# Performance work log

Measured on AMD Instinct MI355X. Metric: run time of the kernel, lower is better.

## Reference

```python
import jax, jax.numpy as jnp
import numpy as np

NORM = 20.0   # from dataset 'NETS'
ALPHA = 1.0
EPS = 1e-12   # torch F.normalize eps


def _l2_normalize(x):
    n = jnp.sqrt(jnp.sum(x * x, axis=-1, keepdims=True))
    return x / jnp.maximum(n, EPS)


def setup_inputs() -> dict:
    key = jax.random.key(0)
    k1, k2, k3, k4, k5 = jax.random.split(key, 5)
    B, P, C = 4096, 32, 512
    predicted_score = jax.random.uniform(k1, (B,), dtype=jnp.float32) * NORM
    targets = jax.random.uniform(k2, (B,), dtype=jnp.float32) * NORM
    feats = jax.random.normal(k3, (B, C), dtype=jnp.float32)
    pivot_features = jax.random.normal(k4, (B, P, C), dtype=jnp.float32)
    pivot_scores = jax.random.uniform(k5, (B, P), dtype=jnp.float32) * NORM
    return {
        "predicted_score": predicted_score,
        "targets": targets,
        "feats": feats,
        "pivot_features": pivot_features,
        "pivot_scores": pivot_scores,
    }


def reference(predicted_score, targets, feats, pivot_features, pivot_scores):
    scale = ALPHA * NORM
    f = _l2_normalize(feats)                      # (B, C)
    pf = _l2_normalize(pivot_features)            # (B, P, C)
    ps = pivot_scores.astype(jnp.float32)         # (B, P)

    # image-text: (B,1,C) @ (B,C,P) -> (B,P)
    it_matches = jnp.einsum('bc,bpc->bp', f, pf)
    it_label = 1.0 - 2.0 * jnp.abs(targets[:, None] - ps) / scale
    image_text_loss = jnp.mean(jnp.abs(it_matches - it_label))

    # image-image: (B,B)
    ii_matches = f @ f.T
    ii_label = 1.0 - 2.0 * jnp.abs(targets[:, None] - targets[None, :]) / scale
    image_image_loss = jnp.mean(jnp.abs(ii_matches - ii_label))

    # text-text: (B,P,P)
    tt_matches = jnp.einsum('bpc,bqc->bpq', pf, pf)
    tt_label = 1.0 - 2.0 * jnp.abs(ps[:, :, None] - ps[:, None, :]) / scale
    text_text_loss = jnp.mean(jnp.abs(tt_matches - tt_label))

    mae_loss = jnp.mean(jnp.abs(predicted_score - targets))

    return (image_image_loss, text_text_loss, image_text_loss, mae_loss)
```

## Files before the change

### kernel.cpp

```cpp
#include <hip/hip_runtime.h>
#include <hip/hip_bf16.h>
#include <stdint.h>

#define B_N 4096
#define P_N 32
#define C_N 512
#define LABC 0.1f
#define N_II 528
#define GRID_TOTAL (N_II * 9)
#define N_TT (GRID_TOTAL - N_II)

typedef float  floatx4 __attribute__((ext_vector_type(4)));
typedef __bf16 bf16x8  __attribute__((ext_vector_type(8)));

__device__ __forceinline__ unsigned short f2bf(float x) {
    return __builtin_bit_cast(unsigned short, __float2bfloat16(x));
}
__device__ __forceinline__ uint4 pack8(const float4& v0, const float4& v1) {
    uint4 pk;
    pk.x = (unsigned)f2bf(v0.x) | ((unsigned)f2bf(v0.y) << 16);
    pk.y = (unsigned)f2bf(v0.z) | ((unsigned)f2bf(v0.w) << 16);
    pk.z = (unsigned)f2bf(v1.x) | ((unsigned)f2bf(v1.y) << 16);
    pk.w = (unsigned)f2bf(v1.z) | ((unsigned)f2bf(v1.w) << 16);
    return pk;
}
__device__ __forceinline__ void bfly_reduce2(float& a, float& b) {
#pragma unroll
    for (int m = 1; m < 64; m <<= 1) {
        a += __shfl_xor(a, m, 64);
        b += __shfl_xor(b, m, 64);
    }
}
__device__ __forceinline__ void bfly_reduce1(float& a) {
#pragma unroll
    for (int m = 1; m < 64; m <<= 1) a += __shfl_xor(a, m, 64);
}

__global__ __launch_bounds__(256) void k_prep(const float* __restrict__ feats,
                                              const float* __restrict__ pred,
                                              const float* __restrict__ targ,
                                              unsigned short* __restrict__ fb,
                                              float* __restrict__ maePart) {
    const int wave = threadIdx.x >> 6, lane = threadIdx.x & 63;
    const int row = blockIdx.x * 4 + wave;
    const float* src = feats + (size_t)row * C_N + lane * 8;
    float4 v0 = *(const float4*)src;
    float4 v1 = *(const float4*)(src + 4);
    float ss = v0.x*v0.x + v0.y*v0.y + v0.z*v0.z + v0.w*v0.w
             + v1.x*v1.x + v1.y*v1.y + v1.z*v1.z + v1.w*v1.w;
    bfly_reduce1(ss);
    const float inv = rsqrtf(fmaxf(ss, 1e-24f));
    float4 n0 = {v0.x*inv, v0.y*inv, v0.z*inv, v0.w*inv};
    float4 n1 = {v1.x*inv, v1.y*inv, v1.z*inv, v1.w*inv};
    *(uint4*)(fb + (size_t)row * C_N + lane * 8) = pack8(n0, n1);

    if (wave == 0) {
        float v = 0.f;
        if (lane < 4) {
            const int r = blockIdx.x * 4 + lane;
            v = fabsf(pred[r] - targ[r]);
        }
        v += __shfl_xor(v, 1, 64);
        v += __shfl_xor(v, 2, 64);
        if (lane == 0) maePart[blockIdx.x] = v;
    }
}

#define APAD 130
struct TTsm {
    unsigned short pfs[64 * 33 * 8];
    float psS[P_N];
    float rdiag[P_N];
    float redT[4], redI[4];
};
struct IIsm {
    unsigned short As[4 * APAD * 8];
    unsigned short Bs[4 * APAD * 8];
    float tm[128], tn[128];
    float red[4];
};
union SMu { TTsm tt; IIsm ii; };

__global__ __launch_bounds__(256) void k_fused(const float* __restrict__ pf_g,
                                               const float* __restrict__ ps_g,
                                               const float* __restrict__ targets,
                                               const unsigned short* __restrict__ fb,
                                               double* __restrict__ partII,
                                               double* __restrict__ partTT,
                                               double* __restrict__ partIT) {
    __shared__ __align__(16) SMu sm;
    const int tid = threadIdx.x, wave = tid >> 6, lane = tid & 63;
    const int quad = lane >> 4, l15 = lane & 15;
    const int bid = blockIdx.x;
    const bool isII = (bid % 9) == 0;

    if (isII) {
        IIsm& S = sm.ii;
        int bm = 0, rem = bid / 9;
        while (rem >= 32 - bm) { rem -= 32 - bm; ++bm; }
        const int bn = bm + rem;
        const int wr = wave >> 1, wc = wave & 1;
        const int mbase = bm * 128, nbase = bn * 128;

        if (tid < 128) S.tm[tid] = targets[mbase + tid];
        else           S.tn[tid - 128] = targets[nbase + tid - 128];

        const int row = tid >> 1, half = tid & 1;
        const unsigned short* aSrc = fb + (size_t)(mbase + row) * C_N + half * 16;
        const unsigned short* bSrc = fb + (size_t)(nbase + row) * C_N + half * 16;
        const int c0 = half * 2, c1 = half * 2 + 1;

        floatx4 accv[16];
#pragma unroll
        for (int i = 0; i < 16; ++i) accv[i] = (floatx4){0.f, 0.f, 0.f, 0.f};

        uint4 a0 = *(const uint4*)(aSrc);
        uint4 a1 = *(const uint4*)(aSrc + 8);
        uint4 b0 = *(const uint4*)(bSrc);
        uint4 b1 = *(const uint4*)(bSrc + 8);

        for (int ks = 0; ks < 16; ++ks) {
            __syncthreads();
            *(uint4*)&S.As[((size_t)c0 * APAD + row) * 8] = a0;
            *(uint4*)&S.As[((size_t)c1 * APAD + row) * 8] = a1;
            *(uint4*)&S.Bs[((size_t)c0 * APAD + row) * 8] = b0;
            *(uint4*)&S.Bs[((size_t)c1 * APAD + row) * 8] = b1;
            __syncthreads();
            if (ks < 15) {
                const int off = (ks + 1) * 32;
                a0 = *(const uint4*)(aSrc + off);
                a1 = *(const uint4*)(aSrc + off + 8);
                b0 = *(const uint4*)(bSrc + off);
                b1 = *(const uint4*)(bSrc + off + 8);
            }
            bf16x8 af[4], bfv[4];
#pragma unroll
            for (int t = 0; t < 4; ++t)
                af[t] = __builtin_bit_cast(bf16x8, *(const uint4*)&S.As[((size_t)quad * APAD + wr * 64 + t * 16 + l15) * 8]);
#pragma unroll
            for (int t = 0; t < 4; ++t)
                bfv[t] = __builtin_bit_cast(bf16x8, *(const uint4*)&S.Bs[((size_t)quad * APAD + wc * 64 + t * 16 + l15) * 8]);
#pragma unroll
            for (int ti = 0; ti < 4; ++ti)
#pragma unroll
                for (int tj = 0; tj < 4; ++tj)
                    accv[ti * 4 + tj] = __builtin_amdgcn_mfma_f32_16x16x32_bf16(af[ti], bfv[tj], accv[ti * 4 + tj], 0, 0, 0);
        }

        float s = 0.f;
#pragma unroll
        for (int ti = 0; ti < 4; ++ti)
#pragma unroll
            for (int tj = 0; tj < 4; ++tj)
#pragma unroll
                for (int r = 0; r < 4; ++r) {
                    const int p = wr * 64 + ti * 16 + quad * 4 + r;
                    const int q = wc * 64 + tj * 16 + l15;
                    const float lab = 1.f - LABC * fabsf(S.tm[p] - S.tn[q]);
                    s += fabsf(accv[ti * 4 + tj][r] - lab);
                }
        if (bm != bn) s *= 2.f;
        bfly_reduce1(s);
        if (lane == 0) S.red[wave] = s;
        __syncthreads();
        if (tid == 0) partII[bid / 9] = (double)(S.red[0] + S.red[1] + S.red[2] + S.red[3]);
    } else {
        const int b = bid - (bid / 9) - 1;
        TTsm& S = sm.tt;
        if (b >= B_N) {
            if (tid == 0) { partTT[b] = 0.0; partIT[b] = 0.0; }
            return;
        }

        const float* base = pf_g + (size_t)b * P_N * C_N;
        uint4 st[16];
#pragma unroll
        for (int i = 0; i < 8; ++i) {
            const float* src = base + (wave * 8 + i) * C_N + lane * 8;
            st[2 * i]     = *(const uint4*)src;
            st[2 * i + 1] = *(const uint4*)(src + 4);
        }
        uint4 fReg = {0u, 0u, 0u, 0u};
        if (wave == 0) fReg = *(const uint4*)(fb + (size_t)b * C_N + lane * 8);
        if (tid < P_N) S.psS[tid] = ps_g[b * P_N + tid];
        const float tb = targets[b];

#pragma unroll
        for (int i = 0; i < 8; ++i) {
            const int r = wave * 8 + i;
            const float4 v0 = __builtin_bit_cast(float4, st[2 * i]);
            const float4 v1 = __builtin_bit_cast(float4, st[2 * i + 1]);
            *(uint4*)&S.pfs[((size_t)lane * 33 + r) * 8] = pack8(v0, v1);
        }
        if (wave == 0) *(uint4*)&S.pfs[((size_t)lane * 33 + 32) * 8] = fReg;
        __syncthreads();

        const int pt = (wave >> 1) * 16, qt = (wave & 1) * 16;
        const bool doF = (wave < 2);
        floatx4 acc4 = {0.f, 0.f, 0.f, 0.f};
        floatx4 accF = {0.f, 0.f, 0.f, 0.f};
        const uint4 zero4 = {0u, 0u, 0u, 0u};
#pragma unroll
        for (int kk = 0; kk < 16; ++kk) {
            const int ch = kk * 4 + quad;
            bf16x8 a = __builtin_bit_cast(bf16x8, *(const uint4*)&S.pfs[((size_t)ch * 33 + pt + l15) * 8]);
            bf16x8 bb = __builtin_bit_cast(bf16x8, *(const uint4*)&S.pfs[((size_t)ch * 33 + qt + l15) * 8]);
            acc4 = __builtin_amdgcn_mfma_f32_16x16x32_bf16(a, bb, acc4, 0, 0, 0);
            if (doF) {
                uint4 fr = *(const uint4*)&S.pfs[((size_t)ch * 33 + 32) * 8];
                bf16x8 af = __builtin_bit_cast(bf16x8, (l15 == 0) ? fr : zero4);
                accF = __builtin_amdgcn_mfma_f32_16x16x32_bf16(af, bb, accF, 0, 0, 0);
            }
        }
        if (pt == qt) {
            if ((l15 >> 2) == quad) S.rdiag[pt + l15] = rsqrtf(fmaxf(acc4[l15 & 3], 1e-24f));
        }
        __syncthreads();

        float tt_sum = 0.f, it_sum = 0.f;
#pragma unroll
        for (int r = 0; r < 4; ++r) {
            const int p = pt + quad * 4 + r;
            const int q = qt + l15;
            const float val = acc4[r] * S.rdiag[p] * S.rdiag[q];
            const float lab = 1.f - LABC * fabsf(S.psS[p] - S.psS[q]);
            tt_sum += fabsf(val - lab);
        }
        if (doF && quad == 0) {
            const int q = qt + l15;
            const float val = accF[0] * S.rdiag[q];
            const float lab = 1.f - LABC * fabsf(tb - S.psS[q]);
            it_sum = fabsf(val - lab);
        }
        bfly_reduce2(tt_sum, it_sum);
        if (lane == 0) { S.redT[wave] = tt_sum; S.redI[wave] = it_sum; }
        __syncthreads();
        if (tid == 0) {
            partTT[b] = (double)(S.redT[0] + S.redT[1] + S.redT[2] + S.redT[3]);
            partIT[b] = (double)(S.redI[0] + S.redI[1] + S.redI[2] + S.redI[3]);
        }
    }
}

__global__ __launch_bounds__(256) void k_final(const double* __restrict__ partII,
                                               const double* __restrict__ partTT,
                                               const double* __restrict__ partIT,
                                               const float* __restrict__ maePart,
                                               float* __restrict__ out) {
    __shared__ double redA[4], redB[4], redC[4];
    __shared__ float redM[4];
    const int tid = threadIdx.x, wave = tid >> 6, lane = tid & 63;

    double sII = 0.0, sTT = 0.0, sIT = 0.0;
    for (int i = tid; i < N_II; i += 256) sII += partII[i];
    for (int i = tid; i < N_TT; i += 256) { sTT += partTT[i]; sIT += partIT[i]; }
    float sM = maePart[tid] + maePart[tid + 256] + maePart[tid + 512] + maePart[tid + 768];

#pragma unroll
    for (int m = 1; m < 64; m <<= 1) {
        sII += __shfl_xor(sII, m, 64);
        sTT += __shfl_xor(sTT, m, 64);
        sIT += __shfl_xor(sIT, m, 64);
        sM  += __shfl_xor(sM, m, 64);
    }
    if (lane == 0) { redA[wave] = sII; redB[wave] = sTT; redC[wave] = sIT; redM[wave] = sM; }
    __syncthreads();
    if (tid == 0) {
        const double ii = redA[0] + redA[1] + redA[2] + redA[3];
        const double tt = redB[0] + redB[1] + redB[2] + redB[3];
        const double it = redC[0] + redC[1] + redC[2] + redC[3];
        out[0] = (float)(ii / (double)((size_t)B_N * B_N));
        out[1] = (float)(tt / (double)((size_t)B_N * P_N * P_N));
        out[2] = (float)(it / (double)((size_t)B_N * P_N));
        out[3] = (redM[0] + redM[1] + redM[2] + redM[3]) * (1.f / B_N);
    }
}

extern "C" void kernel_launch(void* const* d_in, const int* in_sizes, int n_in,
                              void* d_out, int out_size, void* d_ws, size_t ws_size,
                              hipStream_t stream) {
    const float* pred  = (const float*)d_in[0];
    const float* targ  = (const float*)d_in[1];
    const float* feats = (const float*)d_in[2];
    const float* pf    = (const float*)d_in[3];
    const float* ps    = (const float*)d_in[4];
    float* out = (float*)d_out;

    float* maePart      = (float*)d_ws;
    double* partII      = (double*)((char*)d_ws + 4096);
    double* partTT      = (double*)((char*)d_ws + 16384);
    double* partIT      = (double*)((char*)d_ws + 65536);
    unsigned short* fb  = (unsigned short*)((char*)d_ws + 131072);

    k_prep<<<B_N / 4, 256, 0, stream>>>(feats, pred, targ, fb, maePart);
    k_fused<<<GRID_TOTAL, 256, 0, stream>>>(pf, ps, targ, fb, partII, partTT, partIT);
    k_final<<<1, 256, 0, stream>>>(partII, partTT, partIT, maePart, out);
}
```

Baseline: 382.6 us.

## Split fused II/TT kernel into separate image-image and text-text kernels

Replaces the single interleaved kernel, which chose its branch by block index, with two kernels launched back to back: a GEMM-style image-image tile kernel and a per-batch text-text/image-text kernel. Each kernel now allocates only its own shared memory and register budget instead of the union of both, which could raise occupancy, especially for the memory-bound text-text path. The cost is one extra launch and losing the overlap between the compute-heavy II tiles and the bandwidth-heavy TT blocks that interleaving provided.

```diff
diff --git a/kernel.cpp b/kernel.cpp
--- a/kernel.cpp
+++ b/kernel.cpp
@@ -7,8 +7,6 @@
 #define C_N 512
 #define LABC 0.1f
 #define N_II 528
-#define GRID_TOTAL (N_II * 9)
-#define N_TT (GRID_TOTAL - N_II)
 
 typedef float  floatx4 __attribute__((ext_vector_type(4)));
 typedef __bf16 bf16x8  __attribute__((ext_vector_type(8)));
@@ -67,178 +65,168 @@
 }
 
 #define APAD 130
-struct TTsm {
-    unsigned short pfs[64 * 33 * 8];
-    float psS[P_N];
-    float rdiag[P_N];
-    float redT[4], redI[4];
-};
-struct IIsm {
-    unsigned short As[4 * APAD * 8];
-    unsigned short Bs[4 * APAD * 8];
-    float tm[128], tn[128];
-    float red[4];
-};
-union SMu { TTsm tt; IIsm ii; };
-
-__global__ __launch_bounds__(256) void k_fused(const float* __restrict__ pf_g,
-                                               const float* __restrict__ ps_g,
-                                               const float* __restrict__ targets,
-                                               const unsigned short* __restrict__ fb,
-                                               double* __restrict__ partII,
-                                               double* __restrict__ partTT,
-                                               double* __restrict__ partIT) {
-    __shared__ __align__(16) SMu sm;
+__global__ __launch_bounds__(256) void k_ii(const float* __restrict__ targets,
+                                            const unsigned short* __restrict__ fb,
+                                            double* __restrict__ partII) {
+    __shared__ __align__(16) unsigned short As[4 * APAD * 8];
+    __shared__ __align__(16) unsigned short Bs[4 * APAD * 8];
+    __shared__ float tm[128], tn[128];
+    __shared__ float red[4];
+
     const int tid = threadIdx.x, wave = tid >> 6, lane = tid & 63;
     const int quad = lane >> 4, l15 = lane & 15;
-    const int bid = blockIdx.x;
-    const bool isII = (bid % 9) == 0;
-
-    if (isII) {
-        IIsm& S = sm.ii;
-        int bm = 0, rem = bid / 9;
-        while (rem >= 32 - bm) { rem -= 32 - bm; ++bm; }
-        const int bn = bm + rem;
-        const int wr = wave >> 1, wc = wave & 1;
-        const int mbase = bm * 128, nbase = bn * 128;
-
-        if (tid < 128) S.tm[tid] = targets[mbase + tid];
-        else           S.tn[tid - 128] = targets[nbase + tid - 128];
-
-        const int row = tid >> 1, half = tid & 1;
-        const unsigned short* aSrc = fb + (size_t)(mbase + row) * C_N + half * 16;
-        const unsigned short* bSrc = fb + (size_t)(nbase + row) * C_N + half * 16;
-        const int c0 = half * 2, c1 = half * 2 + 1;
-
-        floatx4 accv[16];
-#pragma unroll
-        for (int i = 0; i < 16; ++i) accv[i] = (floatx4){0.f, 0.f, 0.f, 0.f};
-
-        uint4 a0 = *(const uint4*)(aSrc);
-        uint4 a1 = *(const uint4*)(aSrc + 8);
-        uint4 b0 = *(const uint4*)(bSrc);
-        uint4 b1 = *(const uint4*)(bSrc + 8);
-
-        for (int ks = 0; ks < 16; ++ks) {
-            __syncthreads();
-            *(uint4*)&S.As[((size_t)c0 * APAD + row) * 8] = a0;
-            *(uint4*)&S.As[((size_t)c1 * APAD + row) * 8] = a1;
-            *(uint4*)&S.Bs[((size_t)c0 * APAD + row) * 8] = b0;
-            *(uint4*)&S.Bs[((size_t)c1 * APAD + row) * 8] = b1;
-            __syncthreads();
-            if (ks < 15) {
-                const int off = (ks + 1) * 32;
-                a0 = *(const uint4*)(aSrc + off);
-                a1 = *(const uint4*)(aSrc + off + 8);
-                b0 = *(const uint4*)(bSrc + off);
-                b1 = *(const uint4*)(bSrc + off + 8);
+
+    int bm = 0, rem = blockIdx.x;
+    while (rem >= 32 - bm) { rem -= 32 - bm; ++bm; }
+    const int bn = bm + rem;
+    const int wr = wave >> 1, wc = wave & 1;
+    const int mbase = bm * 128, nbase = bn * 128;
+
+    if (tid < 128) tm[tid] = targets[mbase + tid];
+    else           tn[tid - 128] = targets[nbase + tid - 128];
+
+    const int row = tid >> 1, half = tid & 1;
+    const unsigned short* aSrc = fb + (size_t)(mbase + row) * C_N + half * 16;
+    const unsigned short* bSrc = fb + (size_t)(nbase + row) * C_N + half * 16;
+    const int c0 = half * 2, c1 = half * 2 + 1;
+
+    floatx4 accv[16];
+#pragma unroll
+    for (int i = 0; i < 16; ++i) accv[i] = (floatx4){0.f, 0.f, 0.f, 0.f};
+
+    uint4 a0 = *(const uint4*)(aSrc);
+    uint4 a1 = *(const uint4*)(aSrc + 8);
+    uint4 b0 = *(const uint4*)(bSrc);
+    uint4 b1 = *(const uint4*)(bSrc + 8);
+
+    for (int ks = 0; ks < 16; ++ks) {
+        __syncthreads();
+        *(uint4*)&As[((size_t)c0 * APAD + row) * 8] = a0;
+        *(uint4*)&As[((size_t)c1 * APAD + row) * 8] = a1;
+        *(uint4*)&Bs[((size_t)c0 * APAD + row) * 8] = b0;
+        *(uint4*)&Bs[((size_t)c1 * APAD + row) * 8] = b1;
+        __syncthreads();
+        if (ks < 15) {
+            const int off = (ks + 1) * 32;
+            a0 = *(const uint4*)(aSrc + off);
+            a1 = *(const uint4*)(aSrc + off + 8);
+            b0 = *(const uint4*)(bSrc + off);
+            b1 = *(const uint4*)(bSrc + off + 8);
+        }
+        bf16x8 af[4], bfv[4];
+#pragma unroll
+        for (int t = 0; t < 4; ++t)
+            af[t] = __builtin_bit_cast(bf16x8, *(const uint4*)&As[((size_t)quad * APAD + wr * 64 + t * 16 + l15) * 8]);
+#pragma unroll
+        for (int t = 0; t < 4; ++t)
+            bfv[t] = __builtin_bit_cast(bf16x8, *(const uint4*)&Bs[((size_t)quad * APAD + wc * 64 + t * 16 + l15) * 8]);
+#pragma unroll
+        for (int ti = 0; ti < 4; ++ti)
+#pragma unroll
+            for (int tj = 0; tj < 4; ++tj)
+                accv[ti * 4 + tj] = __builtin_amdgcn_mfma_f32_16x16x32_bf16(af[ti], bfv[tj], accv[ti * 4 + tj], 0, 0, 0);
+    }
+
+    float s = 0.f;
+#pragma unroll
+    for (int ti = 0; ti < 4; ++ti)
+#pragma unroll
+        for (int tj = 0; tj < 4; ++tj)
+#pragma unroll
+            for (int r = 0; r < 4; ++r) {
+                const int p = wr * 64 + ti * 16 + quad * 4 + r;
+                const int q = wc * 64 + tj * 16 + l15;
+                const float lab = 1.f - LABC * fabsf(tm[p] - tn[q]);
+                s += fabsf(accv[ti * 4 + tj][r] - lab);
             }
-            bf16x8 af[4], bfv[4];
-#pragma unroll
-            for (int t = 0; t < 4; ++t)
-                af[t] = __builtin_bit_cast(bf16x8, *(const uint4*)&S.As[((size_t)quad * APAD + wr * 64 + t * 16 + l15) * 8]);
-#pragma unroll
-            for (int t = 0; t < 4; ++t)
-                bfv[t] = __builtin_bit_cast(bf16x8, *(const uint4*)&S.Bs[((size_t)quad * APAD + wc * 64 + t * 16 + l15) * 8]);
-#pragma unroll
-            for (int ti = 0; ti < 4; ++ti)
-#pragma unroll
-                for (int tj = 0; tj < 4; ++tj)
-                    accv[ti * 4 + tj] = __builtin_amdgcn_mfma_f32_16x16x32_bf16(af[ti], bfv[tj], accv[ti * 4 + tj], 0, 0, 0);
+    if (bm != bn) s *= 2.f;
+    bfly_reduce1(s);
+    if (lane == 0) red[wave] = s;
+    __syncthreads();
+    if (tid == 0) partII[blockIdx.x] = (double)(red[0] + red[1] + red[2] + red[3]);
+}
+
+__global__ __launch_bounds__(256) void k_tt(const float* __restrict__ pf_g,
+                                            const float* __restrict__ ps_g,
+                                            const float* __restrict__ targets,
+                                            const unsigned short* __restrict__ fb,
+                                            double* __restrict__ partTT,
+                                            double* __restrict__ partIT) {
+    __shared__ __align__(16) unsigned short pfs[64 * 33 * 8];
+    __shared__ float psS[P_N];
+    __shared__ float rdiag[P_N];
+    __shared__ float redT[4], redI[4];
+
+    const int tid = threadIdx.x, wave = tid >> 6, lane = tid & 63;
+    const int quad = lane >> 4, l15 = lane & 15;
+    const int b = blockIdx.x;
+
+    const float* base = pf_g + (size_t)b * P_N * C_N;
+    uint4 st[16];
+#pragma unroll
+    for (int i = 0; i < 8; ++i) {
+        const float* src = base + (wave * 8 + i) * C_N + lane * 8;
+        st[2 * i]     = *(const uint4*)src;
+        st[2 * i + 1] = *(const uint4*)(src + 4);
+    }
+    uint4 fReg = {0u, 0u, 0u, 0u};
+    if (wave == 0) fReg = *(const uint4*)(fb + (size_t)b * C_N + lane * 8);
+    if (tid < P_N) psS[tid] = ps_g[b * P_N + tid];
+    const float tb = targets[b];
+
+#pragma unroll
+    for (int i = 0; i < 8; ++i) {
+        const int r = wave * 8 + i;
+        const float4 v0 = __builtin_bit_cast(float4, st[2 * i]);
+        const float4 v1 = __builtin_bit_cast(float4, st[2 * i + 1]);
+        *(uint4*)&pfs[((size_t)lane * 33 + r) * 8] = pack8(v0, v1);
+    }
+    if (wave == 0) *(uint4*)&pfs[((size_t)lane * 33 + 32) * 8] = fReg;
+    __syncthreads();
+
+    const int pt = (wave >> 1) * 16, qt = (wave & 1) * 16;
+    const bool doF = (wave < 2);
+    floatx4 acc4 = {0.f, 0.f, 0.f, 0.f};
+    floatx4 accF = {0.f, 0.f, 0.f, 0.f};
+    const uint4 zero4 = {0u, 0u, 0u, 0u};
+#pragma unroll
+    for (int kk = 0; kk < 16; ++kk) {
+        const int ch = kk * 4 + quad;
+        bf16x8 a = __builtin_bit_cast(bf16x8, *(const uint4*)&pfs[((size_t)ch * 33 + pt + l15) * 8]);
+        bf16x8 bb = __builtin_bit_cast(bf16x8, *(const uint4*)&pfs[((size_t)ch * 33 + qt + l15) * 8]);
+        acc4 = __builtin_amdgcn_mfma_f32_16x16x32_bf16(a, bb, acc4, 0, 0, 0);
+        if (doF) {
+            uint4 fr = *(const uint4*)&pfs[((size_t)ch * 33 + 32) * 8];
+            bf16x8 af = __builtin_bit_cast(bf16x8, (l15 == 0) ? fr : zero4);
+            accF = __builtin_amdgcn_mfma_f32_16x16x32_bf16(af, bb, accF, 0, 0, 0);
         }
-
-        float s = 0.f;
-#pragma unroll
-        for (int ti = 0; ti < 4; ++ti)
-#pragma unroll
-            for (int tj = 0; tj < 4; ++tj)
-#pragma unroll
-                for (int r = 0; r < 4; ++r) {
-                    const int p = wr * 64 + ti * 16 + quad * 4 + r;
-                    const int q = wc * 64 + tj * 16 + l15;
-                    const float lab = 1.f - LABC * fabsf(S.tm[p] - S.tn[q]);
-                    s += fabsf(accv[ti * 4 + tj][r] - lab);
-                }
-        if (bm != bn) s *= 2.f;
-        bfly_reduce1(s);
-        if (lane == 0) S.red[wave] = s;
-        __syncthreads();
-        if (tid == 0) partII[bid / 9] = (double)(S.red[0] + S.red[1] + S.red[2] + S.red[3]);
-    } else {
-        const int b = bid - (bid / 9) - 1;
-        TTsm& S = sm.tt;
-        if (b >= B_N) {
-            if (tid == 0) { partTT[b] = 0.0; partIT[b] = 0.0; }
-            return;
-        }
-
-        const float* base = pf_g + (size_t)b * P_N * C_N;
-        uint4 st[16];
-#pragma unroll
-        for (int i = 0; i < 8; ++i) {
-            const float* src = base + (wave * 8 + i) * C_N + lane * 8;
-            st[2 * i]     = *(const uint4*)src;
-            st[2 * i + 1] = *(const uint4*)(src + 4);
-        }
-        uint4 fReg = {0u, 0u, 0u, 0u};
-        if (wave == 0) fReg = *(const uint4*)(fb + (size_t)b * C_N + lane * 8);
-        if (tid < P_N) S.psS[tid] = ps_g[b * P_N + tid];
-        const float tb = targets[b];
-
-#pragma unroll
-        for (int i = 0; i < 8; ++i) {
-            const int r = wave * 8 + i;
-            const float4 v0 = __builtin_bit_cast(float4, st[2 * i]);
-            const float4 v1 = __builtin_bit_cast(float4, st[2 * i + 1]);
-            *(uint4*)&S.pfs[((size_t)lane * 33 + r) * 8] = pack8(v0, v1);
-        }
-        if (wave == 0) *(uint4*)&S.pfs[((size_t)lane * 33 + 32) * 8] = fReg;
-        __syncthreads();
-
-        const int pt = (wave >> 1) * 16, qt = (wave & 1) * 16;
-        const bool doF = (wave < 2);
-        floatx4 acc4 = {0.f, 0.f, 0.f, 0.f};
-        floatx4 accF = {0.f, 0.f, 0.f, 0.f};
-        const uint4 zero4 = {0u, 0u, 0u, 0u};
-#pragma unroll
-        for (int kk = 0; kk < 16; ++kk) {
-            const int ch = kk * 4 + quad;
-            bf16x8 a = __builtin_bit_cast(bf16x8, *(const uint4*)&S.pfs[((size_t)ch * 33 + pt + l15) * 8]);
-            bf16x8 bb = __builtin_bit_cast(bf16x8, *(const uint4*)&S.pfs[((size_t)ch * 33 + qt + l15) * 8]);
-            acc4 = __builtin_amdgcn_mfma_f32_16x16x32_bf16(a, bb, acc4, 0, 0, 0);
-            if (doF) {
-                uint4 fr = *(const uint4*)&S.pfs[((size_t)ch * 33 + 32) * 8];
-                bf16x8 af = __builtin_bit_cast(bf16x8, (l15 == 0) ? fr : zero4);
-                accF = __builtin_amdgcn_mfma_f32_16x16x32_bf16(af, bb, accF, 0, 0, 0);
-            }
-        }
-        if (pt == qt) {
-            if ((l15 >> 2) == quad) S.rdiag[pt + l15] = rsqrtf(fmaxf(acc4[l15 & 3], 1e-24f));
-        }
-        __syncthreads();
-
-        float tt_sum = 0.f, it_sum = 0.f;
-#pragma unroll
-        for (int r = 0; r < 4; ++r) {
-            const int p = pt + quad * 4 + r;
-            const int q = qt + l15;
-            const float val = acc4[r] * S.rdiag[p] * S.rdiag[q];
-            const float lab = 1.f - LABC * fabsf(S.psS[p] - S.psS[q]);
-            tt_sum += fabsf(val - lab);
-        }
-        if (doF && quad == 0) {
-            const int q = qt + l15;
-            const float val = accF[0] * S.rdiag[q];
-            const float lab = 1.f - LABC * fabsf(tb - S.psS[q]);
-            it_sum = fabsf(val - lab);
-        }
-        bfly_reduce2(tt_sum, it_sum);
-        if (lane == 0) { S.redT[wave] = tt_sum; S.redI[wave] = it_sum; }
-        __syncthreads();
-        if (tid == 0) {
-            partTT[b] = (double)(S.redT[0] + S.redT[1] + S.redT[2] + S.redT[3]);
-            partIT[b] = (double)(S.redI[0] + S.redI[1] + S.redI[2] + S.redI[3]);
-        }
+    }
+    if (pt == qt) {
+        if ((l15 >> 2) == quad) rdiag[pt + l15] = rsqrtf(fmaxf(acc4[l15 & 3], 1e-24f));
+    }
+    __syncthreads();
+
+    float tt_sum = 0.f, it_sum = 0.f;
+#pragma unroll
+    for (int r = 0; r < 4; ++r) {
+        const int p = pt + quad * 4 + r;
+        const int q = qt + l15;
+        const float val = acc4[r] * rdiag[p] * rdiag[q];
+        const float lab = 1.f - LABC * fabsf(psS[p] - psS[q]);
+        tt_sum += fabsf(val - lab);
+    }
+    if (doF && quad == 0) {
+        const int q = qt + l15;
+        const float val = accF[0] * rdiag[q];
+        const float lab = 1.f - LABC * fabsf(tb - psS[q]);
+        it_sum = fabsf(val - lab);
+    }
+    bfly_reduce2(tt_sum, it_sum);
+    if (lane == 0) { redT[wave] = tt_sum; redI[wave] = it_sum; }
+    __syncthreads();
+    if (tid == 0) {
+        partTT[b] = (double)(redT[0] + redT[1] + redT[2] + redT[3]);
+        partIT[b] = (double)(redI[0] + redI[1] + redI[2] + redI[3]);
     }
 }
 
@@ -253,7 +241,7 @@
 
     double sII = 0.0, sTT = 0.0, sIT = 0.0;
     for (int i = tid; i < N_II; i += 256) sII += partII[i];
-    for (int i = tid; i < N_TT; i += 256) { sTT += partTT[i]; sIT += partIT[i]; }
+    for (int i = tid; i < B_N; i += 256) { sTT += partTT[i]; sIT += partIT[i]; }
     float sM = maePart[tid] + maePart[tid + 256] + maePart[tid + 512] + maePart[tid + 768];
 
 #pragma unroll
@@ -293,6 +281,7 @@
     unsigned short* fb  = (unsigned short*)((char*)d_ws + 131072);
 
     k_prep<<<B_N / 4, 256, 0, stream>>>(feats, pred, targ, fb, maePart);
-    k_fused<<<GRID_TOTAL, 256, 0, stream>>>(pf, ps, targ, fb, partII, partTT, partIT);
+    k_ii<<<N_II, 256, 0, stream>>>(targ, fb, partII);
+    k_tt<<<B_N, 256, 0, stream>>>(pf, ps, targ, fb, partTT, partIT);
     k_final<<<1, 256, 0, stream>>>(partII, partTT, partIT, maePart, out);
 }
```

After: 401.6 us. +5.0%, slower.
